# Optimization experiments

Hardware: AMD Instinct MI355X
Metric: run time of the kernel (lower is better)

## Reference

```python
import jax, jax.numpy as jnp
import numpy as np

DIM = 1024
NUM_HEADS = 16
HEAD_DIM = DIM // NUM_HEADS
SCALE = HEAD_DIM ** -0.5


def setup_inputs() -> dict:
    key = jax.random.key(0)
    k1, k2, k3, k4 = jax.random.split(key, 4)
    x = jax.random.normal(k1, (4, 2048, DIM), dtype=jnp.float32)
    # torch nn.Linear(dim, 3*dim, bias=False): weight shape [3*dim, dim]
    w_qkv = jax.random.normal(k2, (3 * DIM, DIM), dtype=jnp.float32) * (DIM ** -0.5)
    # torch nn.Linear(dim, dim): weight [dim, dim], bias [dim]
    w_proj = jax.random.normal(k3, (DIM, DIM), dtype=jnp.float32) * (DIM ** -0.5)
    b_proj = jax.random.normal(k4, (DIM,), dtype=jnp.float32) * 0.01
    return {"x": x, "w_qkv": w_qkv, "w_proj": w_proj, "b_proj": b_proj}


def reference(x, w_qkv, w_proj, b_proj):
    B, N, C = x.shape
    # qkv: [B, N, 3*C] -> [3, B, H, N, Dh]
    qkv = (x @ w_qkv.T).reshape(B, N, 3, NUM_HEADS, HEAD_DIM)
    qkv = jnp.transpose(qkv, (2, 0, 3, 1, 4))
    q, k, v = qkv[0], qkv[1], qkv[2]
    # full score matrix, as in the original module
    attn = jnp.einsum("bhqd,bhkd->bhqk", q, k) * SCALE
    attn = jax.nn.softmax(attn, axis=-1)
    out = jnp.einsum("bhqk,bhkd->bhqd", attn, v)  # [B,H,N,Dh]
    out = jnp.transpose(out, (0, 2, 1, 3)).reshape(B, N, C)
    return out @ w_proj.T + b_proj
```

## Files before the change

kernel.cpp:

```cpp
#include <hip/hip_runtime.h>
#include <stdint.h>

#define DIM 1024
#define SEQ 2048
#define BATCH 4
#define ROWS (BATCH*SEQ)
#define QSCALE 0.1803368801111f

typedef __attribute__((ext_vector_type(8))) short bf16x8;
typedef __attribute__((ext_vector_type(4))) float f32x4;
typedef __attribute__((ext_vector_type(8))) _Float16 f16x8;
typedef __attribute__((ext_vector_type(2))) __fp16 fp16x2_raw;

#if __has_builtin(__builtin_amdgcn_exp2f)
#define EXP2F(x) __builtin_amdgcn_exp2f(x)
#else
#define EXP2F(x) __expf((x) * 0.69314718056f)
#endif

#define MFMA_BF16_K32(a,b,c) __builtin_amdgcn_mfma_f32_16x16x32_bf16(a,b,c,0,0,0)
#define MFMA_F16_K32(a,b,c)  __builtin_amdgcn_mfma_f32_16x16x32_f16(a,b,c,0,0,0)

__device__ __forceinline__ unsigned short f2bf(float f) {
  union { float f; unsigned int u; } v; v.f = f;
  unsigned int u = v.u;
  return (unsigned short)((u + 0x7FFFu + ((u >> 16) & 1u)) >> 16);
}

__device__ __forceinline__ unsigned short f2h(float f) {
  union { _Float16 h; unsigned short u; } v;
  v.h = (_Float16)f;
  return v.u;
}

__device__ __forceinline__ unsigned int pkrtz_bits(float lo, float hi) {
  union { fp16x2_raw h; unsigned int u; } v;
  v.h = __builtin_amdgcn_cvt_pkrtz(lo, hi);
  return v.u;
}

__device__ __forceinline__ void gload_lds16(const void* g, void* l) {
  __builtin_amdgcn_global_load_lds(
      (const __attribute__((address_space(1))) unsigned int*)g,
      (__attribute__((address_space(3))) unsigned int*)l,
      16, 0, 0);
}

__global__ void cast_all(const float* __restrict__ x,
                         const float* __restrict__ wq,
                         const float* __restrict__ wp,
                         unsigned short* __restrict__ xb,
                         unsigned short* __restrict__ wqb,
                         unsigned short* __restrict__ wpb) {
  const int i = (blockIdx.x * blockDim.x + threadIdx.x) * 4;
  const float* src;
  unsigned short* dst;
  int off;
  if (i < ROWS * DIM)                 { src = x;  dst = xb;  off = i; }
  else if (i < ROWS * DIM + 3 * DIM * DIM) { src = wq; dst = wqb; off = i - ROWS * DIM; }
  else                                { src = wp; dst = wpb; off = i - ROWS * DIM - 3 * DIM * DIM; }
  float4 f = *(const float4*)(src + off);
  ushort4 o;
  o.x = f2bf(f.x); o.y = f2bf(f.y); o.z = f2bf(f.z); o.w = f2bf(f.w);
  *(ushort4*)(dst + off) = o;
}

template<int SWAP>
__device__ __forceinline__ f32x4 mm(bf16x8 a, bf16x8 b, f32x4 c) {
  if constexpr (SWAP) return __builtin_amdgcn_mfma_f32_16x16x32_bf16(b, a, c, 0, 0, 0);
  else                return __builtin_amdgcn_mfma_f32_16x16x32_bf16(a, b, c, 0, 0, 0);
}

template<int SWAP, int NTX>
__global__ __launch_bounds__(512, 2) void gemm_qkv8(
    const unsigned short* __restrict__ A,
    const unsigned short* __restrict__ W,
    unsigned short* __restrict__ qb,
    unsigned short* __restrict__ kb,
    unsigned short* __restrict__ vtb) {
  constexpr int K = DIM;
  constexpr int NT = K / 64;
  constexpr int N0B = SWAP ? 0 : 2048;
  __shared__ unsigned short Al[2][256 * 64];
  __shared__ unsigned short Bl[2][256 * 64];

  const int tid  = threadIdx.x;
  const int wave = tid >> 6, lane = tid & 63;
  const int quad = lane >> 4, l16 = lane & 15;
  const int wm = wave >> 2, wn = wave & 3;

  constexpr int nwg = NTX * 32;
  int id = blockIdx.y * NTX + blockIdx.x;
  id = (id & 7) * (nwg >> 3) + (id >> 3);
  const int bx = id % NTX, by = id / NTX;
  const int m0 = by * 256, n0 = N0B + bx * 256;

  const int srow8 = lane >> 3;
  const int schk  = (lane & 7) ^ srow8;
  const unsigned short* Ast = A + (size_t)(m0 + wave * 8 + srow8) * K + (schk << 3);
  const unsigned short* Bst = W + (size_t)(n0 + wave * 8 + srow8) * K + (schk << 3);

  auto stg = [&](const unsigned short* g, int R0, int kt, unsigned short* l) {
    gload_lds16((const void*)(g + (size_t)R0 * K + kt),
                (void*)(l + (R0 + wave * 8) * 64));
  };
  auto ldf = [&](const unsigned short* base, int rb, int idx, int kk) -> bf16x8 {
    const int r = rb + idx * 16 + l16;
    return *(const bf16x8*)&base[r * 64 + (((kk * 4 + quad) ^ (l16 & 7)) << 3)];
  };

  f32x4 acc[8][4];
#pragma unroll
  for (int i = 0; i < 8; ++i)
#pragma unroll
    for (int j = 0; j < 4; ++j) acc[i][j] = (f32x4)0.f;

  stg(Ast, 0, 0, Al[0]);  stg(Ast, 128, 0, Al[0]);
  stg(Ast, 64, 0, Al[0]); stg(Ast, 192, 0, Al[0]);
  stg(Bst, 0, 0, Bl[0]);  stg(Bst, 64, 0, Bl[0]);
  stg(Bst, 128, 0, Bl[0]); stg(Bst, 192, 0, Bl[0]);
  stg(Ast, 0, 64, Al[1]);  stg(Ast, 128, 64, Al[1]);
  stg(Bst, 0, 64, Bl[1]);  stg(Bst, 64, 64, Bl[1]);
  stg(Ast, 64, 64, Al[1]); stg(Ast, 192, 64, Al[1]);
  asm volatile("s_waitcnt vmcnt(6)" ::: "memory");
  __builtin_amdgcn_s_barrier();

  bf16x8 af[4][2], bf[4][2];
  int buf = 0;
  for (int t = 0; t < NT; ++t, buf ^= 1) {
    const unsigned short* Ac = Al[buf];
    const unsigned short* Bc = Bl[buf];
    unsigned short* Asg = Al[buf];
    unsigned short* Bsg = Bl[buf];
    const int kt2 = (t + 2) * 64;

#pragma unroll
    for (int mi = 0; mi < 4; ++mi) {
      af[mi][0] = ldf(Ac, wm * 128, mi, 0);
      af[mi][1] = ldf(Ac, wm * 128, mi, 1);
    }
#pragma unroll
    for (int ni = 0; ni < 2; ++ni) {
      bf[ni][0] = ldf(Bc, wn * 64, ni, 0);
      bf[ni][1] = ldf(Bc, wn * 64, ni, 1);
    }
    if (t + 1 < NT) {
      stg(Bst, 128, (t + 1) * 64, Bl[buf ^ 1]);
      stg(Bst, 192, (t + 1) * 64, Bl[buf ^ 1]);
    }
    __builtin_amdgcn_s_barrier();
    asm volatile("s_waitcnt lgkmcnt(0)" ::: "memory");
    __builtin_amdgcn_s_setprio(1);
#pragma unroll
    for (int mi = 0; mi < 4; ++mi)
#pragma unroll
      for (int ni = 0; ni < 2; ++ni)
#pragma unroll
        for (int kk = 0; kk < 2; ++kk)
          acc[mi][ni] = mm<SWAP>(af[mi][kk], bf[ni][kk], acc[mi][ni]);
    __builtin_amdgcn_s_setprio(0);
    __builtin_amdgcn_s_barrier();

#pragma unroll
    for (int ni = 2; ni < 4; ++ni) {
      bf[ni][0] = ldf(Bc, wn * 64, ni, 0);
      bf[ni][1] = ldf(Bc, wn * 64, ni, 1);
    }
    if (t + 2 < NT) {
      stg(Ast, 0, kt2, Asg);
      stg(Ast, 128, kt2, Asg);
    }
    __builtin_amdgcn_s_barrier();
    asm volatile("s_waitcnt lgkmcnt(0)" ::: "memory");
    __builtin_amdgcn_s_setprio(1);
#pragma unroll
    for (int mi = 0; mi < 4; ++mi)
#pragma unroll
      for (int ni = 2; ni < 4; ++ni)
#pragma unroll
        for (int kk = 0; kk < 2; ++kk)
          acc[mi][ni] = mm<SWAP>(af[mi][kk], bf[ni][kk], acc[mi][ni]);
    __builtin_amdgcn_s_setprio(0);
    __builtin_amdgcn_s_barrier();

#pragma unroll
    for (int mi = 0; mi < 4; ++mi) {
      af[mi][0] = ldf(Ac, wm * 128, mi + 4, 0);
      af[mi][1] = ldf(Ac, wm * 128, mi + 4, 1);
    }
    if (t + 2 < NT) {
      stg(Bst, 0, kt2, Bsg);
      stg(Bst, 64, kt2, Bsg);
    }
    __builtin_amdgcn_s_barrier();
    asm volatile("s_waitcnt lgkmcnt(0)" ::: "memory");
    __builtin_amdgcn_s_setprio(1);
#pragma unroll
    for (int mi = 0; mi < 4; ++mi)
#pragma unroll
      for (int ni = 2; ni < 4; ++ni)
#pragma unroll
        for (int kk = 0; kk < 2; ++kk)
          acc[mi + 4][ni] = mm<SWAP>(af[mi][kk], bf[ni][kk], acc[mi + 4][ni]);
    __builtin_amdgcn_s_setprio(0);
    __builtin_amdgcn_s_barrier();

    if (t + 2 < NT) {
      stg(Ast, 64, kt2, Asg);
      stg(Ast, 192, kt2, Asg);
      asm volatile("s_waitcnt vmcnt(6)" ::: "memory");
    } else {
      asm volatile("s_waitcnt vmcnt(0)" ::: "memory");
    }
    __builtin_amdgcn_s_barrier();
    __builtin_amdgcn_s_setprio(1);
#pragma unroll
    for (int mi = 0; mi < 4; ++mi)
#pragma unroll
      for (int ni = 0; ni < 2; ++ni)
#pragma unroll
        for (int kk = 0; kk < 2; ++kk)
          acc[mi + 4][ni] = mm<SWAP>(af[mi][kk], bf[ni][kk], acc[mi + 4][ni]);
    __builtin_amdgcn_s_setprio(0);
    __builtin_amdgcn_s_barrier();
  }

  if constexpr (SWAP) {
    const float sc = (n0 < 1024) ? QSCALE : 1.f;
    unsigned short* base = (n0 < 1024) ? qb : kb;
#pragma unroll
    for (int mi = 0; mi < 8; ++mi) {
      const int tok = m0 + wm * 128 + mi * 16 + l16;
      const int b = tok >> 11, n = tok & 2047;
#pragma unroll
      for (int ni = 0; ni < 4; ++ni) {
        const int f0 = n0 + wn * 64 + ni * 16 + quad * 4;
        const int h = (f0 >> 6) & 15, d = f0 & 63;
        ushort4 o4;
        o4.x = f2bf(acc[mi][ni][0] * sc);
        o4.y = f2bf(acc[mi][ni][1] * sc);
        o4.z = f2bf(acc[mi][ni][2] * sc);
        o4.w = f2bf(acc[mi][ni][3] * sc);
        *(ushort4*)&base[((size_t)(b * 16 + h) * SEQ + n) * 64 + d] = o4;
      }
    }
  } else {
#pragma unroll
    for (int mi = 0; mi < 8; ++mi) {
      const int row = m0 + wm * 128 + mi * 16 + quad * 4;
      const int b = row >> 11, n = row & 2047;
#pragma unroll
      for (int ni = 0; ni < 4; ++ni) {
        const int col = n0 + wn * 64 + ni * 16 + l16;
        const int h = (col >> 6) & 15, d = col & 63;
        ushort4 o4;
        o4.x = f2h(acc[mi][ni][0]); o4.y = f2h(acc[mi][ni][1]);
        o4.z = f2h(acc[mi][ni][2]); o4.w = f2h(acc[mi][ni][3]);
        *(ushort4*)&vtb[((size_t)(b * 16 + h) * 64 + d) * SEQ + n] = o4;
      }
    }
  }
}

template<int EPI>
__global__ __launch_bounds__(512, 2) void gemm8_128x256(
    const unsigned short* __restrict__ A,
    const unsigned short* __restrict__ W,
    unsigned short* __restrict__ vtb,
    float* __restrict__ outp,
    const float* __restrict__ bias) {
  constexpr int K = DIM;
  constexpr int NT = K / 64;
  __shared__ unsigned short Al[2][128 * 64];
  __shared__ unsigned short Bl[2][256 * 64];

  const int tid  = threadIdx.x;
  const int wave = tid >> 6, lane = tid & 63;
  const int quad = lane >> 4, l16 = lane & 15;
  const int wm = wave >> 2, wn = wave & 3;

  int id = blockIdx.y * 4 + blockIdx.x;
  id = (id & 7) * 32 + (id >> 3);
  const int bx = id & 3, by = id >> 2;
  const int m0 = by * 128, n0 = bx * 256;

  const int srow8 = lane >> 3;
  const int schk  = (lane & 7) ^ srow8;
  const unsigned short* Ast = A + (size_t)(m0 + srow8) * K + (schk << 3);
  const unsigned short* Bst = W + (size_t)(n0 + srow8) * K + (schk << 3);

  auto stgA = [&](int kt, unsigned short* l, int R0, int R1) {
    const int rs = (wave < 4 ? R0 : R1) + (wave & 3) * 8;
    gload_lds16((const void*)(Ast + (size_t)rs * K + kt), (void*)(l + rs * 64));
  };
  auto stgB = [&](int kt, unsigned short* l, int R0, int R1) {
    const int rs = (wave < 4 ? R0 : R1) + (wave & 3) * 8;
    gload_lds16((const void*)(Bst + (size_t)rs * K + kt), (void*)(l + rs * 64));
  };
  auto ldf = [&](const unsigned short* base, int rb, int idx, int kk) -> bf16x8 {
    const int r = rb + idx * 16 + l16;
    return *(const bf16x8*)&base[r * 64 + (((kk * 4 + quad) ^ (l16 & 7)) << 3)];
  };

  f32x4 acc[4][4];
#pragma unroll
  for (int i = 0; i < 4; ++i)
#pragma unroll
    for (int j = 0; j < 4; ++j) acc[i][j] = (f32x4)0.f;

  stgA(0, Al[0], 0, 64);   stgA(0, Al[0], 32, 96);
  stgB(0, Bl[0], 0, 64);   stgB(0, Bl[0], 32, 96);
  stgB(0, Bl[0], 128, 192); stgB(0, Bl[0], 160, 224);
  stgA(64, Al[1], 0, 64);  stgA(64, Al[1], 32, 96);
  stgB(64, Bl[1], 0, 64);  stgB(64, Bl[1], 32, 96);
  asm volatile("s_waitcnt vmcnt(4)" ::: "memory");
  __builtin_amdgcn_s_barrier();

  bf16x8 af[2][2], bf[4][2];
  int buf = 0;
  for (int t = 0; t < NT; ++t, buf ^= 1) {
    const unsigned short* Ac = Al[buf];
    const unsigned short* Bc = Bl[buf];
    unsigned short* Asg = Al[buf];
    unsigned short* Bsg = Bl[buf];
    const int kt2 = (t + 2) * 64;

#pragma unroll
    for (int i = 0; i < 2; ++i) {
      af[i][0] = ldf(Ac, wm * 64, i, 0);
      af[i][1] = ldf(Ac, wm * 64, i, 1);
    }
#pragma unroll
    for (int ni = 0; ni < 2; ++ni) {
      bf[ni][0] = ldf(Bc, wn * 64, ni, 0);
      bf[ni][1] = ldf(Bc, wn * 64, ni, 1);
    }
    if (t + 1 < NT) {
      stgB((t + 1) * 64, Bl[buf ^ 1], 128, 192);
      stgB((t + 1) * 64, Bl[buf ^ 1], 160, 224);
    }
    __builtin_amdgcn_s_barrier();
    asm volatile("s_waitcnt lgkmcnt(0)" ::: "memory");
    __builtin_amdgcn_s_setprio(1);
#pragma unroll
    for (int mi = 0; mi < 2; ++mi)
#pragma unroll
      for (int ni = 0; ni < 2; ++ni)
#pragma unroll
        for (int kk = 0; kk < 2; ++kk)
          acc[mi][ni] = mm<0>(af[mi][kk], bf[ni][kk], acc[mi][ni]);
    __builtin_amdgcn_s_setprio(0);
    __builtin_amdgcn_s_barrier();

#pragma unroll
    for (int ni = 2; ni < 4; ++ni) {
      bf[ni][0] = ldf(Bc, wn * 64, ni, 0);
      bf[ni][1] = ldf(Bc, wn * 64, ni, 1);
    }
    if (t + 2 < NT) stgA(kt2, Asg, 0, 64);
    __builtin_amdgcn_s_barrier();
    asm volatile("s_waitcnt lgkmcnt(0)" ::: "memory");
    __builtin_amdgcn_s_setprio(1);
#pragma unroll
    for (int mi = 0; mi < 2; ++mi)
#pragma unroll
      for (int ni = 2; ni < 4; ++ni)
#pragma unroll
        for (int kk = 0; kk < 2; ++kk)
          acc[mi][ni] = mm<0>(af[mi][kk], bf[ni][kk], acc[mi][ni]);
    __builtin_amdgcn_s_setprio(0);
    __builtin_amdgcn_s_barrier();

#pragma unroll
    for (int i = 0; i < 2; ++i) {
      af[i][0] = ldf(Ac, wm * 64, i + 2, 0);
      af[i][1] = ldf(Ac, wm * 64, i + 2, 1);
    }
    if (t + 2 < NT) {
      stgB(kt2, Bsg, 0, 64);
      stgB(kt2, Bsg, 32, 96);
    }
    __builtin_amdgcn_s_barrier();
    asm volatile("s_waitcnt lgkmcnt(0)" ::: "memory");
    __builtin_amdgcn_s_setprio(1);
#pragma unroll
    for (int mi = 0; mi < 2; ++mi)
#pragma unroll
      for (int ni = 2; ni < 4; ++ni)
#pragma unroll
        for (int kk = 0; kk < 2; ++kk)
          acc[mi + 2][ni] = mm<0>(af[mi][kk], bf[ni][kk], acc[mi + 2][ni]);
    __builtin_amdgcn_s_setprio(0);
    __builtin_amdgcn_s_barrier();

    if (t + 2 < NT) {
      stgA(kt2, Asg, 32, 96);
      asm volatile("s_waitcnt vmcnt(4)" ::: "memory");
    } else {
      asm volatile("s_waitcnt vmcnt(0)" ::: "memory");
    }
    __builtin_amdgcn_s_barrier();
    __builtin_amdgcn_s_setprio(1);
#pragma unroll
    for (int mi = 0; mi < 2; ++mi)
#pragma unroll
      for (int ni = 0; ni < 2; ++ni)
#pragma unroll
        for (int kk = 0; kk < 2; ++kk)
          acc[mi + 2][ni] = mm<0>(af[mi][kk], bf[ni][kk], acc[mi + 2][ni]);
    __builtin_amdgcn_s_setprio(0);
    __builtin_amdgcn_s_barrier();
  }

  if constexpr (EPI == 0) {
#pragma unroll
    for (int mi = 0; mi < 4; ++mi) {
      const int row = m0 + wm * 64 + mi * 16 + quad * 4;
      const int b = row >> 11, n = row & 2047;
#pragma unroll
      for (int ni = 0; ni < 4; ++ni) {
        const int col = n0 + wn * 64 + ni * 16 + l16;
        const int h = (col >> 6) & 15, d = col & 63;
        ushort4 o4;
        o4.x = f2h(acc[mi][ni][0]); o4.y = f2h(acc[mi][ni][1]);
        o4.z = f2h(acc[mi][ni][2]); o4.w = f2h(acc[mi][ni][3]);
        *(ushort4*)&vtb[((size_t)(b * 16 + h) * 64 + d) * SEQ + n] = o4;
      }
    }
  } else {
#pragma unroll
    for (int mi = 0; mi < 4; ++mi) {
      const int row = m0 + wm * 64 + mi * 16 + quad * 4;
#pragma unroll
      for (int ni = 0; ni < 4; ++ni) {
        const int col = n0 + wn * 64 + ni * 16 + l16;
        const float bv = bias[col];
#pragma unroll
        for (int r = 0; r < 4; ++r)
          outp[(size_t)(row + r) * DIM + col] = acc[mi][ni][r] + bv;
      }
    }
  }
}

__global__ __launch_bounds__(512, 4) void attn_kernel(
    const unsigned short* __restrict__ qb,
    const unsigned short* __restrict__ kb,
    const unsigned short* __restrict__ vtb,
    unsigned short* __restrict__ out) {
  __shared__ unsigned short Kl[2][64 * 64];
  __shared__ unsigned short Vl[2][64 * 64];

  const int tid  = threadIdx.x;
  const int wave = tid >> 6, lane = tid & 63;
  const int quad = lane >> 4, l16 = lane & 15;
  const int bh    = blockIdx.x;
  const int qtile = blockIdx.y;
  const size_t qkbase = (size_t)bh * SEQ * 64;
  const int q0 = qtile * 256 + wave * 32;

  bf16x8 qf[2][2];
#pragma unroll
  for (int mi = 0; mi < 2; mi++)
#pragma unroll
    for (int kk = 0; kk < 2; kk++)
      qf[mi][kk] = *(const bf16x8*)&qb[qkbase + (size_t)(q0 + mi * 16 + l16) * 64 + kk * 32 + quad * 8];

  f32x4 o[2][4];
#pragma unroll
  for (int mi = 0; mi < 2; mi++)
#pragma unroll
    for (int nt = 0; nt < 4; nt++) o[mi][nt] = (f32x4)0.f;
  f32x4 lacc[2];
#pragma unroll
  for (int mi = 0; mi < 2; mi++) lacc[mi] = (f32x4)0.f;

  union { f16x8 v; unsigned int d[4]; } ones8;
#pragma unroll
  for (int j = 0; j < 4; j++) ones8.d[j] = 0x3C003C00u;

  const unsigned short* Kg = kb + qkbase;
  const unsigned short* Vg = vtb + (size_t)bh * 64 * SEQ;
  const int srow = tid >> 3;
  const int schk = tid & 7;
  const int swK = (srow & 3) | (((srow >> 3) & 1) << 2);
  const int swV = srow & 7;

  auto stage = [&](int kt, int b) {
    gload_lds16((const void*)(Kg + (size_t)(kt + srow) * 64 + (schk ^ swK) * 8),
                (void*)&Kl[b][wave * 512]);
    gload_lds16((const void*)(Vg + (size_t)srow * SEQ + kt + (schk ^ swV) * 8),
                (void*)&Vl[b][wave * 512]);
  };

  stage(0, 0);

  const int rbase = ((l16 >> 2) << 3) + (l16 & 3);
  const int sR = (l16 & 3) | (((l16 >> 2) & 1) << 2);

  int buf = 0;
  for (int kt = 0; kt < SEQ; kt += 64, buf ^= 1) {
    __syncthreads();
    if (kt + 64 < SEQ) stage(kt + 64, buf ^ 1);

#pragma unroll
    for (int kk = 0; kk < 2; kk++) {
      bf16x8 kf[2][2];
#pragma unroll
      for (int T = 0; T < 2; T++) {
        const int R = kk * 32 + rbase + 4 * T;
        kf[T][0] = *(const bf16x8*)&Kl[buf][R * 64 + ((quad ^ sR) << 3)];
        kf[T][1] = *(const bf16x8*)&Kl[buf][R * 64 + (((4 + quad) ^ sR) << 3)];
      }
      f16x8 vf[4];
#pragma unroll
      for (int nt = 0; nt < 4; nt++) {
        const int vr = nt * 16 + l16;
        vf[nt] = *(const f16x8*)&Vl[buf][vr * 64 + (((kk * 4 + quad) ^ (vr & 7)) << 3)];
      }
#pragma unroll
      for (int mi = 0; mi < 2; mi++) {
        f32x4 s0 = (f32x4)0.f, s1 = (f32x4)0.f;
        s0 = MFMA_BF16_K32(kf[0][0], qf[mi][0], s0);
        s0 = MFMA_BF16_K32(kf[0][1], qf[mi][1], s0);
        s1 = MFMA_BF16_K32(kf[1][0], qf[mi][0], s1);
        s1 = MFMA_BF16_K32(kf[1][1], qf[mi][1], s1);
        union { f16x8 v; unsigned int d[4]; } pu;
        pu.d[0] = pkrtz_bits(EXP2F(s0[0]), EXP2F(s0[1]));
        pu.d[1] = pkrtz_bits(EXP2F(s0[2]), EXP2F(s0[3]));
        pu.d[2] = pkrtz_bits(EXP2F(s1[0]), EXP2F(s1[1]));
        pu.d[3] = pkrtz_bits(EXP2F(s1[2]), EXP2F(s1[3]));
        lacc[mi] = MFMA_F16_K32(pu.v, ones8.v, lacc[mi]);
#pragma unroll
        for (int nt = 0; nt < 4; nt++)
          o[mi][nt] = MFMA_F16_K32(pu.v, vf[nt], o[mi][nt]);
      }
    }
  }

  const int h = bh & 15, b = bh >> 4;
#pragma unroll
  for (int mi = 0; mi < 2; mi++) {
    float inv[4];
#pragma unroll
    for (int r = 0; r < 4; r++) inv[r] = 1.f / lacc[mi][r];
#pragma unroll
    for (int nt = 0; nt < 4; nt++)
#pragma unroll
      for (int r = 0; r < 4; r++)
        out[((size_t)(b * SEQ + q0 + mi * 16 + quad * 4 + r)) * DIM + h * 64 + nt * 16 + l16] =
            f2bf(o[mi][nt][r] * inv[r]);
  }
}

extern "C" void kernel_launch(void* const* d_in, const int* in_sizes, int n_in,
                              void* d_out, int out_size, void* d_ws, size_t ws_size,
                              hipStream_t stream) {
  const float* x      = (const float*)d_in[0];
  const float* w_qkv  = (const float*)d_in[1];
  const float* w_proj = (const float*)d_in[2];
  const float* b_proj = (const float*)d_in[3];
  float* outp = (float*)d_out;

  char* ws = (char*)d_ws;
  unsigned short* xb     = (unsigned short*)(ws);
  unsigned short* wqkvb  = (unsigned short*)(ws + (16u << 20));
  unsigned short* wprojb = (unsigned short*)(ws + (22u << 20));
  unsigned short* qb     = (unsigned short*)(ws + (24u << 20));
  unsigned short* kb     = (unsigned short*)(ws + (40u << 20));
  unsigned short* vtb    = (unsigned short*)(ws + (56u << 20));
  unsigned short* aout   = (unsigned short*)(ws + (72u << 20));

  const int total4 = (ROWS * DIM + 3 * DIM * DIM + DIM * DIM) / 4;
  cast_all<<<total4 / 256, 256, 0, stream>>>(x, w_qkv, w_proj, xb, wqkvb, wprojb);

  gemm_qkv8<1, 8><<<dim3(8, 32), 512, 0, stream>>>(xb, wqkvb, qb, kb, vtb);
  gemm8_128x256<0><<<dim3(4, 64), 512, 0, stream>>>(
      xb, wqkvb + (size_t)2048 * DIM, vtb, nullptr, nullptr);
  attn_kernel<<<dim3(64, 8), 512, 0, stream>>>(qb, kb, vtb, aout);
  gemm8_128x256<1><<<dim3(4, 64), 512, 0, stream>>>(
      aout, wprojb, nullptr, outp, b_proj);
}
```

Baseline: 257.6 us.

## Load K and V fragments directly from global memory, dropping LDS staging

The attention kernel no longer stages K and V tiles into double-buffered shared memory with async global-to-LDS loads and barriers. Each wave now reads its MFMA fragments straight from global memory (relying on L1/L2 caching, since all waves in a block read the same K/V). This removes the __syncthreads per tile and the LDS traffic, but every wave issues its own redundant global loads and there is no explicit prefetch to hide latency.

```diff
diff --git a/kernel.cpp b/kernel.cpp
--- a/kernel.cpp
+++ b/kernel.cpp
@@ -448,9 +448,6 @@
     const unsigned short* __restrict__ kb,
     const unsigned short* __restrict__ vtb,
     unsigned short* __restrict__ out) {
-  __shared__ unsigned short Kl[2][64 * 64];
-  __shared__ unsigned short Vl[2][64 * 64];
-
   const int tid  = threadIdx.x;
   const int wave = tid >> 6, lane = tid & 63;
   const int quad = lane >> 4, l16 = lane & 15;
@@ -479,45 +476,25 @@
 #pragma unroll
   for (int j = 0; j < 4; j++) ones8.d[j] = 0x3C003C00u;
 
-  const unsigned short* Kg = kb + qkbase;
-  const unsigned short* Vg = vtb + (size_t)bh * 64 * SEQ;
-  const int srow = tid >> 3;
-  const int schk = tid & 7;
-  const int swK = (srow & 3) | (((srow >> 3) & 1) << 2);
-  const int swV = srow & 7;
-
-  auto stage = [&](int kt, int b) {
-    gload_lds16((const void*)(Kg + (size_t)(kt + srow) * 64 + (schk ^ swK) * 8),
-                (void*)&Kl[b][wave * 512]);
-    gload_lds16((const void*)(Vg + (size_t)srow * SEQ + kt + (schk ^ swV) * 8),
-                (void*)&Vl[b][wave * 512]);
-  };
-
-  stage(0, 0);
-
   const int rbase = ((l16 >> 2) << 3) + (l16 & 3);
-  const int sR = (l16 & 3) | (((l16 >> 2) & 1) << 2);
-
-  int buf = 0;
-  for (int kt = 0; kt < SEQ; kt += 64, buf ^= 1) {
-    __syncthreads();
-    if (kt + 64 < SEQ) stage(kt + 64, buf ^ 1);
-
+  const unsigned short* Kp = kb + qkbase + (size_t)rbase * 64 + quad * 8;
+  const unsigned short* Vp = vtb + (size_t)bh * 64 * SEQ + (size_t)l16 * SEQ + quad * 8;
+
+  for (int kt = 0; kt < SEQ; kt += 64) {
 #pragma unroll
     for (int kk = 0; kk < 2; kk++) {
+      const int kOff = (kt + kk * 32) * 64;
+      const int vOff = kt + kk * 32;
       bf16x8 kf[2][2];
 #pragma unroll
       for (int T = 0; T < 2; T++) {
-        const int R = kk * 32 + rbase + 4 * T;
-        kf[T][0] = *(const bf16x8*)&Kl[buf][R * 64 + ((quad ^ sR) << 3)];
-        kf[T][1] = *(const bf16x8*)&Kl[buf][R * 64 + (((4 + quad) ^ sR) << 3)];
+        kf[T][0] = *(const bf16x8*)&Kp[kOff + (4 * T) * 64];
+        kf[T][1] = *(const bf16x8*)&Kp[kOff + (4 * T) * 64 + 32];
       }
       f16x8 vf[4];
 #pragma unroll
-      for (int nt = 0; nt < 4; nt++) {
-        const int vr = nt * 16 + l16;
-        vf[nt] = *(const f16x8*)&Vl[buf][vr * 64 + (((kk * 4 + quad) ^ (vr & 7)) << 3)];
-      }
+      for (int nt = 0; nt < 4; nt++)
+        vf[nt] = *(const f16x8*)&Vp[(size_t)(nt * 16) * SEQ + vOff];
 #pragma unroll
       for (int mi = 0; mi < 2; mi++) {
         f32x4 s0 = (f32x4)0.f, s1 = (f32x4)0.f;
```

After: 415.0 us. +61.1%, slower.

## Merge QKV GEMMs into one launch and triple-buffer attention K/V loads

Applied to the files above, without the earlier changes.

Folds the Q/K projection GEMM and the separate V projection GEMM into a single 12x32-tile kernel. Each block picks the swapped (Q/K) or unswapped (V-transpose) epilogue from its column offset, which removes one launch and the tail of the smaller grid. The attention kernel moves from double to triple buffering of K/V tiles in LDS, waits with explicit vmcnt counts instead of __syncthreads, and raises wave priority around the MFMA blocks. The extra LDS buffer raises shared-memory use per block and may reduce occupancy. The V tiles now use the 256x256 tile shape instead of 128x256.

```diff
diff --git a/kernel.cpp b/kernel.cpp
--- a/kernel.cpp
+++ b/kernel.cpp
@@ -20,6 +20,8 @@
 
 #define MFMA_BF16_K32(a,b,c) __builtin_amdgcn_mfma_f32_16x16x32_bf16(a,b,c,0,0,0)
 #define MFMA_F16_K32(a,b,c)  __builtin_amdgcn_mfma_f32_16x16x32_f16(a,b,c,0,0,0)
+
+template<int N> struct IC { static constexpr int v = N; };
 
 __device__ __forceinline__ unsigned short f2bf(float f) {
   union { float f; unsigned int u; } v; v.f = f;
@@ -71,8 +73,7 @@
   else                return __builtin_amdgcn_mfma_f32_16x16x32_bf16(a, b, c, 0, 0, 0);
 }
 
-template<int SWAP, int NTX>
-__global__ __launch_bounds__(512, 2) void gemm_qkv8(
+__global__ __launch_bounds__(512, 2) void gemm_qkvu(
     const unsigned short* __restrict__ A,
     const unsigned short* __restrict__ W,
     unsigned short* __restrict__ qb,
@@ -80,7 +81,6 @@
     unsigned short* __restrict__ vtb) {
   constexpr int K = DIM;
   constexpr int NT = K / 64;
-  constexpr int N0B = SWAP ? 0 : 2048;
   __shared__ unsigned short Al[2][256 * 64];
   __shared__ unsigned short Bl[2][256 * 64];
 
@@ -89,11 +89,11 @@
   const int quad = lane >> 4, l16 = lane & 15;
   const int wm = wave >> 2, wn = wave & 3;
 
-  constexpr int nwg = NTX * 32;
-  int id = blockIdx.y * NTX + blockIdx.x;
+  constexpr int nwg = 12 * 32;
+  int id = blockIdx.y * 12 + blockIdx.x;
   id = (id & 7) * (nwg >> 3) + (id >> 3);
-  const int bx = id % NTX, by = id / NTX;
-  const int m0 = by * 256, n0 = N0B + bx * 256;
+  const int bx = id % 12, by = id / 12;
+  const int m0 = by * 256, n0 = bx * 256;
 
   const int srow8 = lane >> 3;
   const int schk  = (lane & 7) ^ srow8;
@@ -109,157 +109,164 @@
     return *(const bf16x8*)&base[r * 64 + (((kk * 4 + quad) ^ (l16 & 7)) << 3)];
   };
 
-  f32x4 acc[8][4];
-#pragma unroll
-  for (int i = 0; i < 8; ++i)
-#pragma unroll
-    for (int j = 0; j < 4; ++j) acc[i][j] = (f32x4)0.f;
-
-  stg(Ast, 0, 0, Al[0]);  stg(Ast, 128, 0, Al[0]);
-  stg(Ast, 64, 0, Al[0]); stg(Ast, 192, 0, Al[0]);
-  stg(Bst, 0, 0, Bl[0]);  stg(Bst, 64, 0, Bl[0]);
-  stg(Bst, 128, 0, Bl[0]); stg(Bst, 192, 0, Bl[0]);
-  stg(Ast, 0, 64, Al[1]);  stg(Ast, 128, 64, Al[1]);
-  stg(Bst, 0, 64, Bl[1]);  stg(Bst, 64, 64, Bl[1]);
-  stg(Ast, 64, 64, Al[1]); stg(Ast, 192, 64, Al[1]);
-  asm volatile("s_waitcnt vmcnt(6)" ::: "memory");
-  __builtin_amdgcn_s_barrier();
-
-  bf16x8 af[4][2], bf[4][2];
-  int buf = 0;
-  for (int t = 0; t < NT; ++t, buf ^= 1) {
-    const unsigned short* Ac = Al[buf];
-    const unsigned short* Bc = Bl[buf];
-    unsigned short* Asg = Al[buf];
-    unsigned short* Bsg = Bl[buf];
-    const int kt2 = (t + 2) * 64;
-
-#pragma unroll
-    for (int mi = 0; mi < 4; ++mi) {
-      af[mi][0] = ldf(Ac, wm * 128, mi, 0);
-      af[mi][1] = ldf(Ac, wm * 128, mi, 1);
-    }
-#pragma unroll
-    for (int ni = 0; ni < 2; ++ni) {
-      bf[ni][0] = ldf(Bc, wn * 64, ni, 0);
-      bf[ni][1] = ldf(Bc, wn * 64, ni, 1);
-    }
-    if (t + 1 < NT) {
-      stg(Bst, 128, (t + 1) * 64, Bl[buf ^ 1]);
-      stg(Bst, 192, (t + 1) * 64, Bl[buf ^ 1]);
-    }
-    __builtin_amdgcn_s_barrier();
-    asm volatile("s_waitcnt lgkmcnt(0)" ::: "memory");
-    __builtin_amdgcn_s_setprio(1);
-#pragma unroll
-    for (int mi = 0; mi < 4; ++mi)
-#pragma unroll
-      for (int ni = 0; ni < 2; ++ni)
-#pragma unroll
-        for (int kk = 0; kk < 2; ++kk)
-          acc[mi][ni] = mm<SWAP>(af[mi][kk], bf[ni][kk], acc[mi][ni]);
-    __builtin_amdgcn_s_setprio(0);
-    __builtin_amdgcn_s_barrier();
-
-#pragma unroll
-    for (int ni = 2; ni < 4; ++ni) {
-      bf[ni][0] = ldf(Bc, wn * 64, ni, 0);
-      bf[ni][1] = ldf(Bc, wn * 64, ni, 1);
-    }
-    if (t + 2 < NT) {
-      stg(Ast, 0, kt2, Asg);
-      stg(Ast, 128, kt2, Asg);
-    }
-    __builtin_amdgcn_s_barrier();
-    asm volatile("s_waitcnt lgkmcnt(0)" ::: "memory");
-    __builtin_amdgcn_s_setprio(1);
-#pragma unroll
-    for (int mi = 0; mi < 4; ++mi)
-#pragma unroll
-      for (int ni = 2; ni < 4; ++ni)
-#pragma unroll
-        for (int kk = 0; kk < 2; ++kk)
-          acc[mi][ni] = mm<SWAP>(af[mi][kk], bf[ni][kk], acc[mi][ni]);
-    __builtin_amdgcn_s_setprio(0);
-    __builtin_amdgcn_s_barrier();
-
-#pragma unroll
-    for (int mi = 0; mi < 4; ++mi) {
-      af[mi][0] = ldf(Ac, wm * 128, mi + 4, 0);
-      af[mi][1] = ldf(Ac, wm * 128, mi + 4, 1);
-    }
-    if (t + 2 < NT) {
-      stg(Bst, 0, kt2, Bsg);
-      stg(Bst, 64, kt2, Bsg);
-    }
-    __builtin_amdgcn_s_barrier();
-    asm volatile("s_waitcnt lgkmcnt(0)" ::: "memory");
-    __builtin_amdgcn_s_setprio(1);
-#pragma unroll
-    for (int mi = 0; mi < 4; ++mi)
-#pragma unroll
-      for (int ni = 2; ni < 4; ++ni)
-#pragma unroll
-        for (int kk = 0; kk < 2; ++kk)
-          acc[mi + 4][ni] = mm<SWAP>(af[mi][kk], bf[ni][kk], acc[mi + 4][ni]);
-    __builtin_amdgcn_s_setprio(0);
-    __builtin_amdgcn_s_barrier();
-
-    if (t + 2 < NT) {
-      stg(Ast, 64, kt2, Asg);
-      stg(Ast, 192, kt2, Asg);
-      asm volatile("s_waitcnt vmcnt(6)" ::: "memory");
+  auto body = [&](auto SW) {
+    constexpr int SWAP = decltype(SW)::v;
+
+    f32x4 acc[8][4];
+#pragma unroll
+    for (int i = 0; i < 8; ++i)
+#pragma unroll
+      for (int j = 0; j < 4; ++j) acc[i][j] = (f32x4)0.f;
+
+    stg(Ast, 0, 0, Al[0]);  stg(Ast, 128, 0, Al[0]);
+    stg(Ast, 64, 0, Al[0]); stg(Ast, 192, 0, Al[0]);
+    stg(Bst, 0, 0, Bl[0]);  stg(Bst, 64, 0, Bl[0]);
+    stg(Bst, 128, 0, Bl[0]); stg(Bst, 192, 0, Bl[0]);
+    stg(Ast, 0, 64, Al[1]);  stg(Ast, 128, 64, Al[1]);
+    stg(Bst, 0, 64, Bl[1]);  stg(Bst, 64, 64, Bl[1]);
+    stg(Ast, 64, 64, Al[1]); stg(Ast, 192, 64, Al[1]);
+    asm volatile("s_waitcnt vmcnt(6)" ::: "memory");
+    __builtin_amdgcn_s_barrier();
+
+    bf16x8 af[4][2], bf[4][2];
+    int buf = 0;
+    for (int t = 0; t < NT; ++t, buf ^= 1) {
+      const unsigned short* Ac = Al[buf];
+      const unsigned short* Bc = Bl[buf];
+      unsigned short* Asg = Al[buf];
+      unsigned short* Bsg = Bl[buf];
+      const int kt2 = (t + 2) * 64;
+
+#pragma unroll
+      for (int mi = 0; mi < 4; ++mi) {
+        af[mi][0] = ldf(Ac, wm * 128, mi, 0);
+        af[mi][1] = ldf(Ac, wm * 128, mi, 1);
+      }
+#pragma unroll
+      for (int ni = 0; ni < 2; ++ni) {
+        bf[ni][0] = ldf(Bc, wn * 64, ni, 0);
+        bf[ni][1] = ldf(Bc, wn * 64, ni, 1);
+      }
+      if (t + 1 < NT) {
+        stg(Bst, 128, (t + 1) * 64, Bl[buf ^ 1]);
+        stg(Bst, 192, (t + 1) * 64, Bl[buf ^ 1]);
+      }
+      __builtin_amdgcn_s_barrier();
+      asm volatile("s_waitcnt lgkmcnt(0)" ::: "memory");
+      __builtin_amdgcn_s_setprio(1);
+#pragma unroll
+      for (int mi = 0; mi < 4; ++mi)
+#pragma unroll
+        for (int ni = 0; ni < 2; ++ni)
+#pragma unroll
+          for (int kk = 0; kk < 2; ++kk)
+            acc[mi][ni] = mm<SWAP>(af[mi][kk], bf[ni][kk], acc[mi][ni]);
+      __builtin_amdgcn_s_setprio(0);
+      __builtin_amdgcn_s_barrier();
+
+#pragma unroll
+      for (int ni = 2; ni < 4; ++ni) {
+        bf[ni][0] = ldf(Bc, wn * 64, ni, 0);
+        bf[ni][1] = ldf(Bc, wn * 64, ni, 1);
+      }
+      if (t + 2 < NT) {
+        stg(Ast, 0, kt2, Asg);
+        stg(Ast, 128, kt2, Asg);
+      }
+      __builtin_amdgcn_s_barrier();
+      asm volatile("s_waitcnt lgkmcnt(0)" ::: "memory");
+      __builtin_amdgcn_s_setprio(1);
+#pragma unroll
+      for (int mi = 0; mi < 4; ++mi)
+#pragma unroll
+        for (int ni = 2; ni < 4; ++ni)
+#pragma unroll
+          for (int kk = 0; kk < 2; ++kk)
+            acc[mi][ni] = mm<SWAP>(af[mi][kk], bf[ni][kk], acc[mi][ni]);
+      __builtin_amdgcn_s_setprio(0);
+      __builtin_amdgcn_s_barrier();
+
+#pragma unroll
+      for (int mi = 0; mi < 4; ++mi) {
+        af[mi][0] = ldf(Ac, wm * 128, mi + 4, 0);
+        af[mi][1] = ldf(Ac, wm * 128, mi + 4, 1);
+      }
+      if (t + 2 < NT) {
+        stg(Bst, 0, kt2, Bsg);
+        stg(Bst, 64, kt2, Bsg);
+      }
+      __builtin_amdgcn_s_barrier();
+      asm volatile("s_waitcnt lgkmcnt(0)" ::: "memory");
+      __builtin_amdgcn_s_setprio(1);
+#pragma unroll
+      for (int mi = 0; mi < 4; ++mi)
+#pragma unroll
+        for (int ni = 2; ni < 4; ++ni)
+#pragma unroll
+          for (int kk = 0; kk < 2; ++kk)
+            acc[mi + 4][ni] = mm<SWAP>(af[mi][kk], bf[ni][kk], acc[mi + 4][ni]);
+      __builtin_amdgcn_s_setprio(0);
+      __builtin_amdgcn_s_barrier();
+
+      if (t + 2 < NT) {
+        stg(Ast, 64, kt2, Asg);
+        stg(Ast, 192, kt2, Asg);
+        asm volatile("s_waitcnt vmcnt(6)" ::: "memory");
+      } else {
+        asm volatile("s_waitcnt vmcnt(0)" ::: "memory");
+      }
+      __builtin_amdgcn_s_barrier();
+      __builtin_amdgcn_s_setprio(1);
+#pragma unroll
+      for (int mi = 0; mi < 4; ++mi)
+#pragma unroll
+        for (int ni = 0; ni < 2; ++ni)
+#pragma unroll
+          for (int kk = 0; kk < 2; ++kk)
+            acc[mi + 4][ni] = mm<SWAP>(af[mi][kk], bf[ni][kk], acc[mi + 4][ni]);
+      __builtin_amdgcn_s_setprio(0);
+      __builtin_amdgcn_s_barrier();
+    }
+
+    if constexpr (SWAP) {
+      const float sc = (n0 < 1024) ? QSCALE : 1.f;
+      unsigned short* base = (n0 < 1024) ? qb : kb;
+#pragma unroll
+      for (int mi = 0; mi < 8; ++mi) {
+        const int tok = m0 + wm * 128 + mi * 16 + l16;
+        const int b = tok >> 11, n = tok & 2047;
+#pragma unroll
+        for (int ni = 0; ni < 4; ++ni) {
+          const int f0 = n0 + wn * 64 + ni * 16 + quad * 4;
+          const int h = (f0 >> 6) & 15, d = f0 & 63;
+          ushort4 o4;
+          o4.x = f2bf(acc[mi][ni][0] * sc);
+          o4.y = f2bf(acc[mi][ni][1] * sc);
+          o4.z = f2bf(acc[mi][ni][2] * sc);
+          o4.w = f2bf(acc[mi][ni][3] * sc);
+          *(ushort4*)&base[((size_t)(b * 16 + h) * SEQ + n) * 64 + d] = o4;
+        }
+      }
     } else {
-      asm volatile("s_waitcnt vmcnt(0)" ::: "memory");
-    }
-    __builtin_amdgcn_s_barrier();
-    __builtin_amdgcn_s_setprio(1);
-#pragma unroll
-    for (int mi = 0; mi < 4; ++mi)
-#pragma unroll
-      for (int ni = 0; ni < 2; ++ni)
-#pragma unroll
-        for (int kk = 0; kk < 2; ++kk)
-          acc[mi + 4][ni] = mm<SWAP>(af[mi][kk], bf[ni][kk], acc[mi + 4][ni]);
-    __builtin_amdgcn_s_setprio(0);
-    __builtin_amdgcn_s_barrier();
-  }
-
-  if constexpr (SWAP) {
-    const float sc = (n0 < 1024) ? QSCALE : 1.f;
-    unsigned short* base = (n0 < 1024) ? qb : kb;
-#pragma unroll
-    for (int mi = 0; mi < 8; ++mi) {
-      const int tok = m0 + wm * 128 + mi * 16 + l16;
-      const int b = tok >> 11, n = tok & 2047;
-#pragma unroll
-      for (int ni = 0; ni < 4; ++ni) {
-        const int f0 = n0 + wn * 64 + ni * 16 + quad * 4;
-        const int h = (f0 >> 6) & 15, d = f0 & 63;
-        ushort4 o4;
-        o4.x = f2bf(acc[mi][ni][0] * sc);
-        o4.y = f2bf(acc[mi][ni][1] * sc);
-        o4.z = f2bf(acc[mi][ni][2] * sc);
-        o4.w = f2bf(acc[mi][ni][3] * sc);
-        *(ushort4*)&base[((size_t)(b * 16 + h) * SEQ + n) * 64 + d] = o4;
-      }
-    }
-  } else {
-#pragma unroll
-    for (int mi = 0; mi < 8; ++mi) {
-      const int row = m0 + wm * 128 + mi * 16 + quad * 4;
-      const int b = row >> 11, n = row & 2047;
-#pragma unroll
-      for (int ni = 0; ni < 4; ++ni) {
-        const int col = n0 + wn * 64 + ni * 16 + l16;
-        const int h = (col >> 6) & 15, d = col & 63;
-        ushort4 o4;
-        o4.x = f2h(acc[mi][ni][0]); o4.y = f2h(acc[mi][ni][1]);
-        o4.z = f2h(acc[mi][ni][2]); o4.w = f2h(acc[mi][ni][3]);
-        *(ushort4*)&vtb[((size_t)(b * 16 + h) * 64 + d) * SEQ + n] = o4;
-      }
-    }
-  }
+#pragma unroll
+      for (int mi = 0; mi < 8; ++mi) {
+        const int row = m0 + wm * 128 + mi * 16 + quad * 4;
+        const int b = row >> 11, n = row & 2047;
+#pragma unroll
+        for (int ni = 0; ni < 4; ++ni) {
+          const int col = n0 + wn * 64 + ni * 16 + l16;
+          const int h = (col >> 6) & 15, d = col & 63;
+          ushort4 o4;
+          o4.x = f2h(acc[mi][ni][0]); o4.y = f2h(acc[mi][ni][1]);
+          o4.z = f2h(acc[mi][ni][2]); o4.w = f2h(acc[mi][ni][3]);
+          *(ushort4*)&vtb[((size_t)(b * 16 + h) * 64 + d) * SEQ + n] = o4;
+        }
+      }
+    }
+  };
+
+  if (n0 < 2048) body(IC<1>{});
+  else           body(IC<0>{});
 }
 
 template<int EPI>
@@ -448,8 +455,8 @@
     const unsigned short* __restrict__ kb,
     const unsigned short* __restrict__ vtb,
     unsigned short* __restrict__ out) {
-  __shared__ unsigned short Kl[2][64 * 64];
-  __shared__ unsigned short Vl[2][64 * 64];
+  __shared__ unsigned short Kl[3][64 * 64];
+  __shared__ unsigned short Vl[3][64 * 64];
 
   const int tid  = threadIdx.x;
   const int wave = tid >> 6, lane = tid & 63;
@@ -494,14 +501,20 @@
   };
 
   stage(0, 0);
+  stage(64, 1);
 
   const int rbase = ((l16 >> 2) << 3) + (l16 & 3);
   const int sR = (l16 & 3) | (((l16 >> 2) & 1) << 2);
 
-  int buf = 0;
-  for (int kt = 0; kt < SEQ; kt += 64, buf ^= 1) {
-    __syncthreads();
-    if (kt + 64 < SEQ) stage(kt + 64, buf ^ 1);
+  int b0 = 0, b1 = 1, b2 = 2;
+  for (int t = 0; t < 32; ++t) {
+    if (t < 31) asm volatile("s_waitcnt vmcnt(2) lgkmcnt(0)" ::: "memory");
+    else        asm volatile("s_waitcnt vmcnt(0) lgkmcnt(0)" ::: "memory");
+    __builtin_amdgcn_s_barrier();
+    if (t + 2 < 32) stage((t + 2) * 64, b2);
+
+    const unsigned short* Kc = &Kl[b0][0];
+    const unsigned short* Vc = &Vl[b0][0];
 
 #pragma unroll
     for (int kk = 0; kk < 2; kk++) {
@@ -509,15 +522,16 @@
 #pragma unroll
       for (int T = 0; T < 2; T++) {
         const int R = kk * 32 + rbase + 4 * T;
-        kf[T][0] = *(const bf16x8*)&Kl[buf][R * 64 + ((quad ^ sR) << 3)];
-        kf[T][1] = *(const bf16x8*)&Kl[buf][R * 64 + (((4 + quad) ^ sR) << 3)];
+        kf[T][0] = *(const bf16x8*)&Kc[R * 64 + ((quad ^ sR) << 3)];
+        kf[T][1] = *(const bf16x8*)&Kc[R * 64 + (((4 + quad) ^ sR) << 3)];
       }
       f16x8 vf[4];
 #pragma unroll
       for (int nt = 0; nt < 4; nt++) {
         const int vr = nt * 16 + l16;
-        vf[nt] = *(const f16x8*)&Vl[buf][vr * 64 + (((kk * 4 + quad) ^ (vr & 7)) << 3)];
-      }
+        vf[nt] = *(const f16x8*)&Vc[vr * 64 + (((kk * 4 + quad) ^ (vr & 7)) << 3)];
+      }
+      __builtin_amdgcn_s_setprio(1);
 #pragma unroll
       for (int mi = 0; mi < 2; mi++) {
         f32x4 s0 = (f32x4)0.f, s1 = (f32x4)0.f;
@@ -535,7 +549,9 @@
         for (int nt = 0; nt < 4; nt++)
           o[mi][nt] = MFMA_F16_K32(pu.v, vf[nt], o[mi][nt]);
       }
-    }
+      __builtin_amdgcn_s_setprio(0);
+    }
+    const int tmp = b0; b0 = b1; b1 = b2; b2 = tmp;
   }
 
   const int h = bh & 15, b = bh >> 4;
@@ -574,9 +590,7 @@
   const int total4 = (ROWS * DIM + 3 * DIM * DIM + DIM * DIM) / 4;
   cast_all<<<total4 / 256, 256, 0, stream>>>(x, w_qkv, w_proj, xb, wqkvb, wprojb);
 
-  gemm_qkv8<1, 8><<<dim3(8, 32), 512, 0, stream>>>(xb, wqkvb, qb, kb, vtb);
-  gemm8_128x256<0><<<dim3(4, 64), 512, 0, stream>>>(
-      xb, wqkvb + (size_t)2048 * DIM, vtb, nullptr, nullptr);
+  gemm_qkvu<<<dim3(12, 32), 512, 0, stream>>>(xb, wqkvb, qb, kb, vtb);
   attn_kernel<<<dim3(64, 8), 512, 0, stream>>>(qb, kb, vtb, aout);
   gemm8_128x256<1><<<dim3(4, 64), 512, 0, stream>>>(
       aout, wprojb, nullptr, outp, b_proj);
```

Result: slower. 264.5 us (+2.7%).
